# Kernel optimization log

Hardware: AMD Instinct MI355X
Metric: run time of the kernel (lower is better)

## Reference

```python
import jax, jax.numpy as jnp
import numpy as np

N = 50000
E = 400000
IN_DIM = 128
OUT_DIM = 512
NUM_MASK = 15000


def _init_linear(key, din, dout):
    s = 1.0 / np.sqrt(din)
    return jax.random.uniform(key, (din, dout), jnp.float32, -s, s)


def setup_inputs() -> dict:
    key = jax.random.key(0)
    ks = jax.random.split(key, 20)
    attr = jax.random.normal(ks[0], (N, IN_DIM), jnp.float32)
    src = jax.random.randint(ks[1], (E,), 0, N, jnp.int32)
    dst = jax.random.randint(ks[2], (E,), 0, N, jnp.int32)
    mask_nodes = jax.random.randint(ks[3], (NUM_MASK,), 0, N, jnp.int32)
    mask_token = jnp.zeros((1, IN_DIM), jnp.float32)
    dims = [(IN_DIM, OUT_DIM), (OUT_DIM, OUT_DIM), (OUT_DIM, OUT_DIM), (OUT_DIM, IN_DIM)]
    params = {}
    for i, (din, dout) in enumerate(dims, start=1):
        params[f"w_self{i}"] = _init_linear(ks[3 * i + 1], din, dout)
        params[f"w_neigh{i}"] = _init_linear(ks[3 * i + 2], din, dout)
        params[f"b{i}"] = jnp.zeros((dout,), jnp.float32)
    return dict(attr=attr, mask_token=mask_token, src=src, dst=dst, mask_nodes=mask_nodes, **params)


def sage_conv(h, src, dst, w_self, w_neigh, b):
    # mean aggregation over in-neighbors (DGL SAGEConv, aggregator_type='mean')
    msg = h[src]                                              # [E, d]
    agg = jax.ops.segment_sum(msg, dst, num_segments=N)       # [N, d]
    deg = jax.ops.segment_sum(jnp.ones((E,), h.dtype), dst, num_segments=N)
    h_neigh = agg / jnp.maximum(deg, 1.0)[:, None]
    return h @ w_self + h_neigh @ w_neigh + b


def reference(attr, mask_token, src, dst, mask_nodes,
              w_self1, w_neigh1, b1, w_self2, w_neigh2, b2,
              w_self3, w_neigh3, b3, w_self4, w_neigh4, b4):
    # mask node features with the mask token
    h = attr.at[mask_nodes].set(mask_token[0])
    h = jax.nn.relu(sage_conv(h, src, dst, w_self1, w_neigh1, b1))
    h = sage_conv(h, src, dst, w_self2, w_neigh2, b2)          # encoded
    h = jax.nn.relu(sage_conv(h, src, dst, w_self3, w_neigh3, b3))
    decoded = sage_conv(h, src, dst, w_self4, w_neigh4, b4)
    x_orig = attr[mask_nodes]
    x_rec = decoded[mask_nodes]
    return jnp.mean((x_rec - x_orig) ** 2)
```

## Files before the change

### kernel.cpp

```cpp
#include <hip/hip_runtime.h>
#include <cstdint>
#include <cstddef>

#define IN_DIM 128
#define HID    512

typedef unsigned int   uint32;
typedef unsigned short u16;
typedef __attribute__((ext_vector_type(8))) short bf16x8;
typedef __attribute__((ext_vector_type(4))) float f32x4;

static inline int imin_h(int a, int b) { return a < b ? a : b; }

__device__ __forceinline__ float bfu2f(uint32 u) { return __uint_as_float(u << 16); }
__device__ __forceinline__ u16 f2bf(float f) {
  uint32 x = __float_as_uint(f);
  x += 0x7fffu + ((x >> 16) & 1u);
  return (u16)(x >> 16);
}
__device__ __forceinline__ uint32 pack2(float a, float b) {
  return (uint32)f2bf(a) | ((uint32)f2bf(b) << 16);
}

#define GLOBAL_AS(p) ((const __attribute__((address_space(1))) void*)(p))
#define LDS_AS(p)    ((__attribute__((address_space(3))) void*)(p))

__global__ void k_zero2(int* __restrict__ a, int na, int* __restrict__ b, int nb) {
  const int total = na + nb;
  for (int i = blockIdx.x * blockDim.x + threadIdx.x; i < total; i += gridDim.x * blockDim.x) {
    if (i < na) a[i] = 0;
    else        b[i - na] = 0;
  }
}

struct WtJobs {
  const float* W[8];
  u16* Wt[8];
  int K[8];
  int Nn[8];
  int start[9];
};

__global__ __launch_bounds__(256)
void k_prep1(const int* __restrict__ dst, int* __restrict__ deg, int E,
             const float4* __restrict__ attr4, uint2* __restrict__ h0, int n4,
             WtJobs jobs) {
  const int wtot = jobs.start[8];
  const int total = E + n4 + wtot;
  for (int i = blockIdx.x * blockDim.x + threadIdx.x; i < total; i += gridDim.x * blockDim.x) {
    if (i < E) {
      atomicAdd(&deg[dst[i]], 1);
    } else if (i < E + n4) {
      const int t = i - E;
      const float4 v = attr4[t];
      h0[t] = make_uint2(pack2(v.x, v.y), pack2(v.z, v.w));
    } else {
      const int t = i - E - n4;
      int s = 0;
#pragma unroll
      for (int j = 0; j < 7; ++j) s += (t >= jobs.start[j + 1]) ? 1 : 0;
      const int loc = t - jobs.start[s];
      const int K = jobs.K[s], Nn = jobs.Nn[s];
      const int n = loc / K, k = loc - n * K;
      const size_t idx = ((size_t)(n >> 4) * (K >> 5) + (k >> 5)) * 512 +
                         ((k >> 3) & 3) * 128 + ((n & 15) << 3) + (k & 7);
      jobs.Wt[s][idx] = f2bf(jobs.W[s][(size_t)k * Nn + n]);
    }
  }
}

__global__ __launch_bounds__(256)
void k_scan1(const int* __restrict__ deg, int* __restrict__ bsum, int n) {
  __shared__ int sm[256];
  const int base = blockIdx.x * 2048 + threadIdx.x * 8;
  int s = 0;
  if (base + 8 <= n) {
    const uint4 a = *reinterpret_cast<const uint4*>(deg + base);
    const uint4 b = *reinterpret_cast<const uint4*>(deg + base + 4);
    s = (int)(a.x + a.y + a.z + a.w + b.x + b.y + b.z + b.w);
  } else {
    for (int i = 0; i < 8; ++i) if (base + i < n) s += deg[base + i];
  }
  sm[threadIdx.x] = s;
  __syncthreads();
  for (int off = 128; off > 0; off >>= 1) {
    if (threadIdx.x < off) sm[threadIdx.x] += sm[threadIdx.x + off];
    __syncthreads();
  }
  if (threadIdx.x == 0) bsum[blockIdx.x] = sm[0];
}

__global__ __launch_bounds__(256)
void k_scan2(int* __restrict__ bsum, int nb, int* __restrict__ rowptr, int n) {
  __shared__ int sm[256];
  const int v = (threadIdx.x < nb) ? bsum[threadIdx.x] : 0;
  sm[threadIdx.x] = v;
  __syncthreads();
  for (int off = 1; off < 256; off <<= 1) {
    const int t = (threadIdx.x >= off) ? sm[threadIdx.x - off] : 0;
    __syncthreads();
    sm[threadIdx.x] += t;
    __syncthreads();
  }
  if (threadIdx.x < nb) bsum[threadIdx.x] = sm[threadIdx.x] - v;
  if (threadIdx.x == nb - 1) rowptr[n] = sm[threadIdx.x];
}

__global__ __launch_bounds__(256)
void k_scan3(const int* __restrict__ deg, const int* __restrict__ bsum,
             int* __restrict__ rowptr, int* __restrict__ cursor, int n) {
  __shared__ int sm[256];
  const int base = blockIdx.x * 2048 + threadIdx.x * 8;
  int v[8];
  int s = 0;
#pragma unroll
  for (int i = 0; i < 8; ++i) {
    v[i] = (base + i < n) ? deg[base + i] : 0;
    s += v[i];
  }
  sm[threadIdx.x] = s;
  __syncthreads();
  for (int off = 1; off < 256; off <<= 1) {
    const int t = (threadIdx.x >= off) ? sm[threadIdx.x - off] : 0;
    __syncthreads();
    sm[threadIdx.x] += t;
    __syncthreads();
  }
  int run = bsum[blockIdx.x] + sm[threadIdx.x] - s;
#pragma unroll
  for (int i = 0; i < 8; ++i) {
    if (base + i < n) { rowptr[base + i] = run; cursor[base + i] = run; }
    run += v[i];
  }
}

__global__ void k_fillmask(const int* __restrict__ src, const int* __restrict__ dst,
                           int* __restrict__ cursor, int* __restrict__ col, int E,
                           const float4* __restrict__ token, const int* __restrict__ mask,
                           uint2* __restrict__ h0, int NM) {
  const int mtot = NM * (IN_DIM / 4);
  const int total = E + mtot;
  for (int i = blockIdx.x * blockDim.x + threadIdx.x; i < total; i += gridDim.x * blockDim.x) {
    if (i < E) {
      const int p = atomicAdd(&cursor[dst[i]], 1);
      col[p] = src[i];
    } else {
      const int t = i - E;
      const int m = t >> 5;
      const int c = t & 31;
      const float4 tv = token[c];
      h0[(size_t)mask[m] * (IN_DIM / 4) + c] = make_uint2(pack2(tv.x, tv.y), pack2(tv.z, tv.w));
    }
  }
}

template <int D, bool REMAP>
__global__ __launch_bounds__(256)
void k_agg(const u16* __restrict__ h, const int* __restrict__ col,
           const int* __restrict__ rowptr, const int* __restrict__ nodes,
           u16* __restrict__ out, int n) {
  constexpr int V = D / 64;
  const int w = blockIdx.x * (blockDim.x >> 6) + (threadIdx.x >> 6);
  if (w >= n) return;
  const int node = REMAP ? nodes[w] : w;
  const int lane = threadIdx.x & 63;
  const int beg = rowptr[node], end = rowptr[node + 1];
  const size_t loff = (size_t)lane * V;
  float acc[V];
#pragma unroll
  for (int j = 0; j < V; ++j) acc[j] = 0.f;

  if constexpr (V == 8) {
    auto L = [&](int e) {
      return *reinterpret_cast<const uint4*>(h + (size_t)col[e] * D + loff);
    };
    for (int e = beg; e < end; e += 8) {
      uint4 c0{}, c1{}, c2{}, c3{}, c4{}, c5{}, c6{}, c7{};
      c0 = L(e);
      if (e + 1 < end) c1 = L(e + 1);
      if (e + 2 < end) c2 = L(e + 2);
      if (e + 3 < end) c3 = L(e + 3);
      if (e + 4 < end) c4 = L(e + 4);
      if (e + 5 < end) c5 = L(e + 5);
      if (e + 6 < end) c6 = L(e + 6);
      if (e + 7 < end) c7 = L(e + 7);
#define ADD4(cv)                                                      \
      acc[0] += bfu2f(cv.x & 0xffffu); acc[1] += bfu2f(cv.x >> 16);   \
      acc[2] += bfu2f(cv.y & 0xffffu); acc[3] += bfu2f(cv.y >> 16);   \
      acc[4] += bfu2f(cv.z & 0xffffu); acc[5] += bfu2f(cv.z >> 16);   \
      acc[6] += bfu2f(cv.w & 0xffffu); acc[7] += bfu2f(cv.w >> 16);
      ADD4(c0) ADD4(c1) ADD4(c2) ADD4(c3) ADD4(c4) ADD4(c5) ADD4(c6) ADD4(c7)
#undef ADD4
    }
  } else {
    auto L = [&](int e) {
      return *reinterpret_cast<const uint32*>(h + (size_t)col[e] * D + loff);
    };
    for (int e = beg; e < end; e += 8) {
      uint32 c0 = 0, c1 = 0, c2 = 0, c3 = 0, c4 = 0, c5 = 0, c6 = 0, c7 = 0;
      c0 = L(e);
      if (e + 1 < end) c1 = L(e + 1);
      if (e + 2 < end) c2 = L(e + 2);
      if (e + 3 < end) c3 = L(e + 3);
      if (e + 4 < end) c4 = L(e + 4);
      if (e + 5 < end) c5 = L(e + 5);
      if (e + 6 < end) c6 = L(e + 6);
      if (e + 7 < end) c7 = L(e + 7);
#define ADD2(cv) acc[0] += bfu2f(cv & 0xffffu); acc[1] += bfu2f(cv >> 16);
      ADD2(c0) ADD2(c1) ADD2(c2) ADD2(c3) ADD2(c4) ADD2(c5) ADD2(c6) ADD2(c7)
#undef ADD2
    }
  }

  const float inv = 1.0f / fmaxf((float)(end - beg), 1.0f);
  u16* o = out + (size_t)w * D + loff;
  if constexpr (V == 8) {
    uint4 u;
    u.x = pack2(acc[0] * inv, acc[1] * inv);
    u.y = pack2(acc[2] * inv, acc[3] * inv);
    u.z = pack2(acc[4] * inv, acc[5] * inv);
    u.w = pack2(acc[6] * inv, acc[7] * inv);
    *reinterpret_cast<uint4*>(o) = u;
  } else {
    *reinterpret_cast<uint32*>(o) = pack2(acc[0] * inv, acc[1] * inv);
  }
}

template <int DIN, bool RELU>
__global__ __launch_bounds__(512, 4)
void k_gemm_big(const u16* __restrict__ A1, const u16* __restrict__ A2,
                const u16* __restrict__ Wt1, const u16* __restrict__ Wt2,
                const float* __restrict__ bias, u16* __restrict__ out, int M) {
  constexpr int DOUT = HID;
  __shared__ char lds[73728];
  constexpr int KS = DIN / 32;
  constexpr int S  = 2 * KS;
  const int tid = threadIdx.x;
  const int w = tid >> 6, l = tid & 63;
  const int l15 = l & 15, l4 = l >> 4;
  const int wm = w >> 2, wn = w & 3;

  const int nwg  = gridDim.x * gridDim.y;
  const int orig = blockIdx.x + gridDim.x * blockIdx.y;
  const int q = nwg >> 3, r = nwg & 7;
  const int xcd = orig & 7, seq = orig >> 3;
  const int wg = (xcd < r ? xcd * (q + 1) : r * (q + 1) + (xcd - r) * q) + seq;
  const int mt = wg >> 1, nt = wg & 1;
  const int m0 = mt * 128, n0 = nt * 256;

  f32x4 acc[4][4];
#pragma unroll
  for (int i = 0; i < 4; ++i)
#pragma unroll
    for (int j = 0; j < 4; ++j) acc[i][j] = (f32x4){0.f, 0.f, 0.f, 0.f};

  const int arow = min(m0 + w * 16 + l15, M - 1);
  const int kl = l4 * 8;
  const u16* pA1 = A1 + (size_t)arow * DIN + kl;
  const u16* pA2 = A2 + (size_t)arow * DIN + kl;
  const u16* bb1 = Wt1 + ((size_t)(n0 >> 4) + 2 * w) * KS * 512 + (size_t)l * 8;
  const u16* bb2 = Wt2 + ((size_t)(n0 >> 4) + 2 * w) * KS * 512 + (size_t)l * 8;

  auto stage = [&](int s) {
    const int ph = s / KS;
    const int kf = s - ph * KS;
    char* buf = lds + (s % 3) * 24576;
    const u16* a0 = (ph ? pA2 : pA1) + kf * 32;
    const u16* b0 = (ph ? bb2 : bb1) + kf * 512;
    const u16* b1 = b0 + KS * 512;
    __builtin_amdgcn_global_load_lds(GLOBAL_AS(a0), LDS_AS(buf + w * 1024), 16, 0, 0);
    __builtin_amdgcn_global_load_lds(GLOBAL_AS(b0), LDS_AS(buf + 8192 + (2 * w + 0) * 1024), 16, 0, 0);
    __builtin_amdgcn_global_load_lds(GLOBAL_AS(b1), LDS_AS(buf + 8192 + (2 * w + 1) * 1024), 16, 0, 0);
  };

  stage(0);
  stage(1);

#pragma unroll
  for (int s = 0; s < S; ++s) {
    if (s + 1 < S) asm volatile("s_waitcnt vmcnt(3)" ::: "memory");
    else           asm volatile("s_waitcnt vmcnt(0)" ::: "memory");
    __builtin_amdgcn_s_barrier();
    if (s + 2 < S) stage(s + 2);
    char* buf = lds + (s % 3) * 24576;
    bf16x8 af[4], bfr[4];
#pragma unroll
    for (int i = 0; i < 4; ++i)
      af[i] = *reinterpret_cast<const bf16x8*>(buf + (wm * 4 + i) * 1024 + l * 16);
#pragma unroll
    for (int j = 0; j < 4; ++j)
      bfr[j] = *reinterpret_cast<const bf16x8*>(buf + 8192 + (wn * 4 + j) * 1024 + l * 16);
#pragma unroll
    for (int i = 0; i < 4; ++i)
#pragma unroll
      for (int j = 0; j < 4; ++j)
        acc[i][j] = __builtin_amdgcn_mfma_f32_16x16x32_bf16(af[i], bfr[j], acc[i][j], 0, 0, 0);
    asm volatile("s_waitcnt lgkmcnt(0)" ::: "memory");
  }
  __builtin_amdgcn_s_barrier();

  u16* eb = (u16*)(lds + w * 9216);
  float bv[4];
#pragma unroll
  for (int j = 0; j < 4; ++j) bv[j] = bias[n0 + wn * 64 + j * 16 + l15];
#pragma unroll
  for (int i = 0; i < 4; ++i)
#pragma unroll
    for (int j = 0; j < 4; ++j)
#pragma unroll
      for (int r = 0; r < 4; ++r) {
        const int lr = i * 16 + l4 * 4 + r;
        float t = acc[i][j][r] + bv[j];
        if (RELU) t = fmaxf(t, 0.f);
        eb[lr * 72 + j * 16 + l15] = f2bf(t);
      }
  asm volatile("s_waitcnt lgkmcnt(0)" ::: "memory");
#pragma unroll
  for (int p = 0; p < 8; ++p) {
    const int lr = p * 8 + (l >> 3);
    const int row = m0 + wm * 64 + lr;
    if (row < M) {
      const uint4 v = *reinterpret_cast<const uint4*>(eb + lr * 72 + (l & 7) * 8);
      *reinterpret_cast<uint4*>(out + (size_t)row * DOUT + n0 + wn * 64 + (l & 7) * 8) = v;
    }
  }
}

template <int DIN, int DOUT>
__global__ __launch_bounds__(256, 3)
void k_gemm_loss(const u16* __restrict__ A1, const u16* __restrict__ A2,
                 const u16* __restrict__ Wt1, const u16* __restrict__ Wt2,
                 const float* __restrict__ bias, const float* __restrict__ attr,
                 float* __restrict__ partials, int M, const int* __restrict__ remap) {
  __shared__ char lds[49152];
  constexpr int KS = DIN / 32;
  constexpr int S  = 2 * KS;
  const int tid = threadIdx.x;
  const int w = tid >> 6, l = tid & 63;
  const int l15 = l & 15, l4 = l >> 4;
  const int wm = w >> 1, wn = w & 1;

  const int nwg  = gridDim.x * gridDim.y;
  const int orig = blockIdx.x + gridDim.x * blockIdx.y;
  const int q = nwg >> 3, r = nwg & 7;
  const int xcd = orig & 7, seq = orig >> 3;
  const int wg = (xcd < r ? xcd * (q + 1) : r * (q + 1) + (xcd - r) * q) + seq;
  constexpr int NT = DOUT / 128;
  const int mt = wg / NT, nt = wg - mt * NT;
  const int m0 = mt * 128, n0 = nt * 128;

  f32x4 acc[4][4];
#pragma unroll
  for (int i = 0; i < 4; ++i)
#pragma unroll
    for (int j = 0; j < 4; ++j) acc[i][j] = (f32x4){0.f, 0.f, 0.f, 0.f};

  const int am0 = min(m0 + (2 * w) * 16 + l15, M - 1);
  const int am1 = min(m0 + (2 * w + 1) * 16 + l15, M - 1);
  const int ar0 = remap[am0];
  const int ar1 = remap[am1];
  const int kl = l4 * 8;
  const u16* pA1r0 = A1 + (size_t)ar0 * DIN + kl;
  const u16* pA1r1 = A1 + (size_t)ar1 * DIN + kl;
  const u16* pA2r0 = A2 + (size_t)am0 * DIN + kl;
  const u16* pA2r1 = A2 + (size_t)am1 * DIN + kl;
  const u16* bb1 = Wt1 + ((size_t)(n0 >> 4) + 2 * w) * KS * 512 + (size_t)l * 8;
  const u16* bb2 = Wt2 + ((size_t)(n0 >> 4) + 2 * w) * KS * 512 + (size_t)l * 8;

  auto stage = [&](int s) {
    const int ph = s / KS;
    const int kf = s - ph * KS;
    char* buf = lds + (s % 3) * 16384;
    const u16* a0 = (ph ? pA2r0 : pA1r0) + kf * 32;
    const u16* a1 = (ph ? pA2r1 : pA1r1) + kf * 32;
    const u16* b0 = (ph ? bb2 : bb1) + kf * 512;
    const u16* b1 = b0 + KS * 512;
    __builtin_amdgcn_global_load_lds(GLOBAL_AS(a0), LDS_AS(buf + (2 * w + 0) * 1024), 16, 0, 0);
    __builtin_amdgcn_global_load_lds(GLOBAL_AS(a1), LDS_AS(buf + (2 * w + 1) * 1024), 16, 0, 0);
    __builtin_amdgcn_global_load_lds(GLOBAL_AS(b0), LDS_AS(buf + 8192 + (2 * w + 0) * 1024), 16, 0, 0);
    __builtin_amdgcn_global_load_lds(GLOBAL_AS(b1), LDS_AS(buf + 8192 + (2 * w + 1) * 1024), 16, 0, 0);
  };

  stage(0);
  stage(1);

#pragma unroll
  for (int s = 0; s < S; ++s) {
    if (s + 1 < S) asm volatile("s_waitcnt vmcnt(4)" ::: "memory");
    else           asm volatile("s_waitcnt vmcnt(0)" ::: "memory");
    __builtin_amdgcn_s_barrier();
    if (s + 2 < S) stage(s + 2);
    char* buf = lds + (s % 3) * 16384;
    bf16x8 af[4], bfr[4];
#pragma unroll
    for (int i = 0; i < 4; ++i)
      af[i] = *reinterpret_cast<const bf16x8*>(buf + (wm * 4 + i) * 1024 + l * 16);
#pragma unroll
    for (int j = 0; j < 4; ++j)
      bfr[j] = *reinterpret_cast<const bf16x8*>(buf + 8192 + (wn * 4 + j) * 1024 + l * 16);
#pragma unroll
    for (int i = 0; i < 4; ++i)
#pragma unroll
      for (int j = 0; j < 4; ++j)
        acc[i][j] = __builtin_amdgcn_mfma_f32_16x16x32_bf16(af[i], bfr[j], acc[i][j], 0, 0, 0);
    asm volatile("s_waitcnt lgkmcnt(0)" ::: "memory");
  }

  float lsum = 0.f;
#pragma unroll
  for (int j = 0; j < 4; ++j) {
    const int c = n0 + wn * 64 + j * 16 + l15;
    const float bv = bias[c];
#pragma unroll
    for (int i = 0; i < 4; ++i) {
      const int rowb = m0 + wm * 64 + i * 16 + l4 * 4;
#pragma unroll
      for (int r2 = 0; r2 < 4; ++r2) {
        const int row = rowb + r2;
        if (row < M) {
          const float t = bfu2f((uint32)f2bf(acc[i][j][r2] + bv));
          const float d = t - attr[(size_t)remap[row] * IN_DIM + c];
          lsum += d * d;
        }
      }
    }
  }
  __syncthreads();
  float* sm = (float*)lds;
  sm[tid] = lsum;
  __syncthreads();
  for (int off2 = 128; off2 > 0; off2 >>= 1) {
    if (tid < off2) sm[tid] += sm[tid + off2];
    __syncthreads();
  }
  if (tid == 0) atomicAdd(&partials[0], sm[0]);
}

__global__ void k_final(const float* __restrict__ partials, float* __restrict__ out, float inv) {
  out[0] = partials[0] * inv;
}

extern "C" void kernel_launch(void* const* d_in, const int* in_sizes, int n_in,
                              void* d_out, int out_size, void* d_ws, size_t ws_size,
                              hipStream_t stream) {
  const float* attr  = (const float*)d_in[0];
  const float* token = (const float*)d_in[1];
  const int*   src   = (const int*)d_in[2];
  const int*   dst   = (const int*)d_in[3];
  const int*   mask  = (const int*)d_in[4];
  const float* Wself[4]  = {(const float*)d_in[5], (const float*)d_in[8],
                            (const float*)d_in[11], (const float*)d_in[14]};
  const float* Wneigh[4] = {(const float*)d_in[6], (const float*)d_in[9],
                            (const float*)d_in[12], (const float*)d_in[15]};
  const float* Bias[4]   = {(const float*)d_in[7], (const float*)d_in[10],
                            (const float*)d_in[13], (const float*)d_in[16]};
  const int N  = in_sizes[0] / IN_DIM;
  const int E  = in_sizes[2];
  const int NM = in_sizes[4];

  size_t off = 0;
  auto take = [&](size_t bytes) -> void* {
    void* p = (char*)d_ws + off;
    off += (bytes + 255) & ~(size_t)255;
    return p;
  };
  u16* HA = (u16*)take((size_t)N * HID * sizeof(u16));
  u16* HB = (u16*)take((size_t)N * HID * sizeof(u16));
  const int dims_in[4]  = {IN_DIM, HID, HID, HID};
  const int dims_out[4] = {HID, HID, HID, IN_DIM};
  u16* WtS[4]; u16* WtN[4];
  for (int i = 0; i < 4; ++i) {
    WtS[i] = (u16*)take((size_t)dims_in[i] * dims_out[i] * sizeof(u16));
    WtN[i] = (u16*)take((size_t)dims_in[i] * dims_out[i] * sizeof(u16));
  }
  int* deg    = (int*)take((size_t)N * sizeof(int));
  int* rowptr = (int*)take((size_t)(N + 1) * sizeof(int));
  int* cursor = (int*)take((size_t)N * sizeof(int));
  int* col    = (int*)take((size_t)E * sizeof(int));
  int* bsum   = (int*)take(256 * sizeof(int));
  float* partials = (float*)take(512 * sizeof(float));

  size_t rem = (ws_size > off + 4096) ? (ws_size - off - 4096) : 0;
  const int cap = (int)(rem / ((size_t)HID * sizeof(u16)));
  const int want = (N + 255) & ~255;
  int chunk = (cap >= want) ? want : (cap & ~255);
  if (chunk < 2048) chunk = 2048;
  u16* CH = (u16*)take((size_t)chunk * HID * sizeof(u16));

  k_zero2<<<imin_h((N + 512 + 255) / 256, 1024), 256, 0, stream>>>(deg, N, (int*)partials, 512);

  WtJobs jobs;
  int acc0 = 0;
  for (int i = 0; i < 4; ++i) {
    jobs.W[2 * i] = Wself[i];  jobs.Wt[2 * i] = WtS[i];
    jobs.K[2 * i] = dims_in[i]; jobs.Nn[2 * i] = dims_out[i];
    jobs.start[2 * i] = acc0;   acc0 += dims_in[i] * dims_out[i];
    jobs.W[2 * i + 1] = Wneigh[i]; jobs.Wt[2 * i + 1] = WtN[i];
    jobs.K[2 * i + 1] = dims_in[i]; jobs.Nn[2 * i + 1] = dims_out[i];
    jobs.start[2 * i + 1] = acc0;  acc0 += dims_in[i] * dims_out[i];
  }
  jobs.start[8] = acc0;
  const int n4 = N * (IN_DIM / 4);
  const int p1 = E + n4 + acc0;
  k_prep1<<<imin_h((p1 + 255) / 256, 4096), 256, 0, stream>>>(
      dst, deg, E, (const float4*)attr, (uint2*)HA, n4, jobs);

  const int nb = (N + 2047) / 2048;
  k_scan1<<<nb, 256, 0, stream>>>(deg, bsum, N);
  k_scan2<<<1, 256, 0, stream>>>(bsum, nb, rowptr, N);
  k_scan3<<<nb, 256, 0, stream>>>(deg, bsum, rowptr, cursor, N);

  const int p2 = E + NM * (IN_DIM / 4);
  k_fillmask<<<imin_h((p2 + 255) / 256, 4096), 256, 0, stream>>>(
      src, dst, cursor, col, E, (const float4*)token, mask, (uint2*)HA, NM);

  auto run_layer = [&](const u16* hin, u16* hout, int din, int layer, bool relu) {
    for (int c0 = 0; c0 < N; c0 += chunk) {
      const int mc = imin_h(chunk, N - c0);
      const int ab = (mc + 3) / 4;
      if (din == IN_DIM)
        k_agg<IN_DIM, false><<<ab, 256, 0, stream>>>(hin, col, rowptr + c0, nullptr, CH, mc);
      else
        k_agg<HID, false><<<ab, 256, 0, stream>>>(hin, col, rowptr + c0, nullptr, CH, mc);
      const u16* a1 = hin + (size_t)c0 * din;
      u16* o = hout + (size_t)c0 * HID;
      const int mb = (mc + 127) / 128;
      if (din == IN_DIM && relu)
        k_gemm_big<IN_DIM, true><<<dim3(2, mb), 512, 0, stream>>>(
            a1, CH, WtS[layer], WtN[layer], Bias[layer], o, mc);
      else if (relu)
        k_gemm_big<HID, true><<<dim3(2, mb), 512, 0, stream>>>(
            a1, CH, WtS[layer], WtN[layer], Bias[layer], o, mc);
      else
        k_gemm_big<HID, false><<<dim3(2, mb), 512, 0, stream>>>(
            a1, CH, WtS[layer], WtN[layer], Bias[layer], o, mc);
    }
  };

  run_layer(HA, HB, IN_DIM, 0, true);
  run_layer(HB, HA, HID,    1, false);
  run_layer(HA, HB, HID,    2, true);

  k_agg<HID, true><<<(NM + 3) / 4, 256, 0, stream>>>(HB, col, rowptr, mask, CH, NM);
  k_gemm_loss<HID, IN_DIM><<<dim3(1, (NM + 127) / 128), 256, 0, stream>>>(
      HB, CH, WtS[3], WtN[3], Bias[3], attr, partials, NM, mask);

  k_final<<<1, 1, 0, stream>>>(partials, (float*)d_out, 1.0f / ((float)NM * IN_DIM));
}
```

Measured before the change: 431.4 us.

## Switch big GEMM to 32x32x16 MFMA with matching weight layout

Rewrites the main layer GEMM to use 32x32x16 bf16 MFMA tiles instead of 16x16x32. Each wave now holds a 2x2 grid of 32x32 accumulators, and the A and B LDS fragment layouts change to match. Weights are pre-transposed into a new 32-column blocked layout. Separate copies in the old 16-row layout are added for the loss GEMM, which still uses the smaller instruction. The aim is fewer MFMA issues and LDS reads per FLOP, at the cost of extra weight-preparation work and a more complex epilogue index mapping.

```diff
diff --git a/kernel.cpp b/kernel.cpp
--- a/kernel.cpp
+++ b/kernel.cpp
@@ -7,8 +7,9 @@
 
 typedef unsigned int   uint32;
 typedef unsigned short u16;
-typedef __attribute__((ext_vector_type(8))) short bf16x8;
-typedef __attribute__((ext_vector_type(4))) float f32x4;
+typedef __attribute__((ext_vector_type(8)))  short bf16x8;
+typedef __attribute__((ext_vector_type(4)))  float f32x4;
+typedef __attribute__((ext_vector_type(16))) float f32x16;
 
 static inline int imin_h(int a, int b) { return a < b ? a : b; }
 
@@ -34,18 +35,19 @@
 }
 
 struct WtJobs {
-  const float* W[8];
-  u16* Wt[8];
-  int K[8];
-  int Nn[8];
-  int start[9];
+  const float* W[10];
+  u16* Wt[10];
+  int K[10];
+  int Nn[10];
+  int mode[10];
+  int start[11];
 };
 
 __global__ __launch_bounds__(256)
 void k_prep1(const int* __restrict__ dst, int* __restrict__ deg, int E,
              const float4* __restrict__ attr4, uint2* __restrict__ h0, int n4,
              WtJobs jobs) {
-  const int wtot = jobs.start[8];
+  const int wtot = jobs.start[10];
   const int total = E + n4 + wtot;
   for (int i = blockIdx.x * blockDim.x + threadIdx.x; i < total; i += gridDim.x * blockDim.x) {
     if (i < E) {
@@ -58,12 +60,17 @@
       const int t = i - E - n4;
       int s = 0;
 #pragma unroll
-      for (int j = 0; j < 7; ++j) s += (t >= jobs.start[j + 1]) ? 1 : 0;
+      for (int j = 0; j < 9; ++j) s += (t >= jobs.start[j + 1]) ? 1 : 0;
       const int loc = t - jobs.start[s];
       const int K = jobs.K[s], Nn = jobs.Nn[s];
       const int n = loc / K, k = loc - n * K;
-      const size_t idx = ((size_t)(n >> 4) * (K >> 5) + (k >> 5)) * 512 +
-                         ((k >> 3) & 3) * 128 + ((n & 15) << 3) + (k & 7);
+      size_t idx;
+      if (jobs.mode[s] == 0)
+        idx = ((size_t)(n >> 5) * (K >> 4) + (k >> 4)) * 512 +
+              ((k >> 3) & 1) * 256 + ((n & 31) << 3) + (k & 7);
+      else
+        idx = ((size_t)(n >> 4) * (K >> 5) + (k >> 5)) * 512 +
+              ((k >> 3) & 3) * 128 + ((n & 15) << 3) + (k & 7);
       jobs.Wt[s][idx] = f2bf(jobs.W[s][(size_t)k * Nn + n]);
     }
   }
@@ -233,11 +240,12 @@
                 const float* __restrict__ bias, u16* __restrict__ out, int M) {
   constexpr int DOUT = HID;
   __shared__ char lds[73728];
-  constexpr int KS = DIN / 32;
-  constexpr int S  = 2 * KS;
+  constexpr int KS   = DIN / 32;
+  constexpr int S    = 2 * KS;
+  constexpr int KS16 = DIN / 16;
   const int tid = threadIdx.x;
   const int w = tid >> 6, l = tid & 63;
-  const int l15 = l & 15, l4 = l >> 4;
+  const int l31 = l & 31, l5 = l >> 5;
   const int wm = w >> 2, wn = w & 3;
 
   const int nwg  = gridDim.x * gridDim.y;
@@ -248,29 +256,30 @@
   const int mt = wg >> 1, nt = wg & 1;
   const int m0 = mt * 128, n0 = nt * 256;
 
-  f32x4 acc[4][4];
-#pragma unroll
-  for (int i = 0; i < 4; ++i)
-#pragma unroll
-    for (int j = 0; j < 4; ++j) acc[i][j] = (f32x4){0.f, 0.f, 0.f, 0.f};
-
-  const int arow = min(m0 + w * 16 + l15, M - 1);
-  const int kl = l4 * 8;
-  const u16* pA1 = A1 + (size_t)arow * DIN + kl;
-  const u16* pA2 = A2 + (size_t)arow * DIN + kl;
-  const u16* bb1 = Wt1 + ((size_t)(n0 >> 4) + 2 * w) * KS * 512 + (size_t)l * 8;
-  const u16* bb2 = Wt2 + ((size_t)(n0 >> 4) + 2 * w) * KS * 512 + (size_t)l * 8;
+  f32x16 acc[2][2];
+#pragma unroll
+  for (int i = 0; i < 2; ++i)
+#pragma unroll
+    for (int j = 0; j < 2; ++j)
+#pragma unroll
+      for (int r2 = 0; r2 < 16; ++r2) acc[i][j][r2] = 0.f;
+
+  const int arow = min(m0 + (w >> 1) * 32 + l31, M - 1);
+  const int kA = (w & 1) * 16 + l5 * 8;
+  const u16* pA1 = A1 + (size_t)arow * DIN + kA;
+  const u16* pA2 = A2 + (size_t)arow * DIN + kA;
+  const u16* bb1 = Wt1 + ((size_t)(n0 >> 5) + w) * KS16 * 512 + (size_t)l * 8;
+  const u16* bb2 = Wt2 + ((size_t)(n0 >> 5) + w) * KS16 * 512 + (size_t)l * 8;
 
   auto stage = [&](int s) {
     const int ph = s / KS;
     const int kf = s - ph * KS;
     char* buf = lds + (s % 3) * 24576;
-    const u16* a0 = (ph ? pA2 : pA1) + kf * 32;
-    const u16* b0 = (ph ? bb2 : bb1) + kf * 512;
-    const u16* b1 = b0 + KS * 512;
-    __builtin_amdgcn_global_load_lds(GLOBAL_AS(a0), LDS_AS(buf + w * 1024), 16, 0, 0);
-    __builtin_amdgcn_global_load_lds(GLOBAL_AS(b0), LDS_AS(buf + 8192 + (2 * w + 0) * 1024), 16, 0, 0);
-    __builtin_amdgcn_global_load_lds(GLOBAL_AS(b1), LDS_AS(buf + 8192 + (2 * w + 1) * 1024), 16, 0, 0);
+    const u16* a = (ph ? pA2 : pA1) + kf * 32;
+    const u16* b = (ph ? bb2 : bb1) + (size_t)(kf * 2) * 512;
+    __builtin_amdgcn_global_load_lds(GLOBAL_AS(a),       LDS_AS(buf + w * 1024), 16, 0, 0);
+    __builtin_amdgcn_global_load_lds(GLOBAL_AS(b),       LDS_AS(buf + 8192 + (2 * w + 0) * 1024), 16, 0, 0);
+    __builtin_amdgcn_global_load_lds(GLOBAL_AS(b + 512), LDS_AS(buf + 8192 + (2 * w + 1) * 1024), 16, 0, 0);
   };
 
   stage(0);
@@ -283,36 +292,42 @@
     __builtin_amdgcn_s_barrier();
     if (s + 2 < S) stage(s + 2);
     char* buf = lds + (s % 3) * 24576;
-    bf16x8 af[4], bfr[4];
-#pragma unroll
-    for (int i = 0; i < 4; ++i)
-      af[i] = *reinterpret_cast<const bf16x8*>(buf + (wm * 4 + i) * 1024 + l * 16);
-#pragma unroll
-    for (int j = 0; j < 4; ++j)
-      bfr[j] = *reinterpret_cast<const bf16x8*>(buf + 8192 + (wn * 4 + j) * 1024 + l * 16);
-#pragma unroll
-    for (int i = 0; i < 4; ++i)
-#pragma unroll
-      for (int j = 0; j < 4; ++j)
-        acc[i][j] = __builtin_amdgcn_mfma_f32_16x16x32_bf16(af[i], bfr[j], acc[i][j], 0, 0, 0);
+    bf16x8 af[2][2], bfr[2][2];
+#pragma unroll
+    for (int i = 0; i < 2; ++i)
+#pragma unroll
+      for (int kk = 0; kk < 2; ++kk)
+        af[i][kk] = *reinterpret_cast<const bf16x8*>(buf + ((wm * 2 + i) * 2 + kk) * 1024 + l * 16);
+#pragma unroll
+    for (int j = 0; j < 2; ++j)
+#pragma unroll
+      for (int kk = 0; kk < 2; ++kk)
+        bfr[j][kk] = *reinterpret_cast<const bf16x8*>(buf + 8192 + ((wn * 2 + j) * 2 + kk) * 1024 + l * 16);
+#pragma unroll
+    for (int kk = 0; kk < 2; ++kk)
+#pragma unroll
+      for (int i = 0; i < 2; ++i)
+#pragma unroll
+        for (int j = 0; j < 2; ++j)
+          acc[i][j] = __builtin_amdgcn_mfma_f32_32x32x16_bf16(af[i][kk], bfr[j][kk], acc[i][j], 0, 0, 0);
     asm volatile("s_waitcnt lgkmcnt(0)" ::: "memory");
   }
   __builtin_amdgcn_s_barrier();
 
   u16* eb = (u16*)(lds + w * 9216);
-  float bv[4];
-#pragma unroll
-  for (int j = 0; j < 4; ++j) bv[j] = bias[n0 + wn * 64 + j * 16 + l15];
-#pragma unroll
-  for (int i = 0; i < 4; ++i)
-#pragma unroll
-    for (int j = 0; j < 4; ++j)
-#pragma unroll
-      for (int r = 0; r < 4; ++r) {
-        const int lr = i * 16 + l4 * 4 + r;
-        float t = acc[i][j][r] + bv[j];
+  float bv[2];
+#pragma unroll
+  for (int j = 0; j < 2; ++j) bv[j] = bias[n0 + wn * 64 + j * 32 + l31];
+#pragma unroll
+  for (int i = 0; i < 2; ++i)
+#pragma unroll
+    for (int j = 0; j < 2; ++j)
+#pragma unroll
+      for (int r2 = 0; r2 < 16; ++r2) {
+        const int lr = i * 32 + (r2 & 3) + 8 * (r2 >> 2) + 4 * l5;
+        float t = acc[i][j][r2] + bv[j];
         if (RELU) t = fmaxf(t, 0.f);
-        eb[lr * 72 + j * 16 + l15] = f2bf(t);
+        eb[lr * 72 + j * 32 + l31] = f2bf(t);
       }
   asm volatile("s_waitcnt lgkmcnt(0)" ::: "memory");
 #pragma unroll
@@ -473,6 +488,8 @@
     WtS[i] = (u16*)take((size_t)dims_in[i] * dims_out[i] * sizeof(u16));
     WtN[i] = (u16*)take((size_t)dims_in[i] * dims_out[i] * sizeof(u16));
   }
+  u16* WtS16_3 = (u16*)take((size_t)HID * IN_DIM * sizeof(u16));
+  u16* WtN16_3 = (u16*)take((size_t)HID * IN_DIM * sizeof(u16));
   int* deg    = (int*)take((size_t)N * sizeof(int));
   int* rowptr = (int*)take((size_t)(N + 1) * sizeof(int));
   int* cursor = (int*)take((size_t)N * sizeof(int));
@@ -493,13 +510,17 @@
   int acc0 = 0;
   for (int i = 0; i < 4; ++i) {
     jobs.W[2 * i] = Wself[i];  jobs.Wt[2 * i] = WtS[i];
-    jobs.K[2 * i] = dims_in[i]; jobs.Nn[2 * i] = dims_out[i];
+    jobs.K[2 * i] = dims_in[i]; jobs.Nn[2 * i] = dims_out[i]; jobs.mode[2 * i] = 0;
     jobs.start[2 * i] = acc0;   acc0 += dims_in[i] * dims_out[i];
     jobs.W[2 * i + 1] = Wneigh[i]; jobs.Wt[2 * i + 1] = WtN[i];
-    jobs.K[2 * i + 1] = dims_in[i]; jobs.Nn[2 * i + 1] = dims_out[i];
+    jobs.K[2 * i + 1] = dims_in[i]; jobs.Nn[2 * i + 1] = dims_out[i]; jobs.mode[2 * i + 1] = 0;
     jobs.start[2 * i + 1] = acc0;  acc0 += dims_in[i] * dims_out[i];
   }
-  jobs.start[8] = acc0;
+  jobs.W[8] = Wself[3];  jobs.Wt[8] = WtS16_3; jobs.K[8] = HID; jobs.Nn[8] = IN_DIM;
+  jobs.mode[8] = 1; jobs.start[8] = acc0; acc0 += HID * IN_DIM;
+  jobs.W[9] = Wneigh[3]; jobs.Wt[9] = WtN16_3; jobs.K[9] = HID; jobs.Nn[9] = IN_DIM;
+  jobs.mode[9] = 1; jobs.start[9] = acc0; acc0 += HID * IN_DIM;
+  jobs.start[10] = acc0;
   const int n4 = N * (IN_DIM / 4);
   const int p1 = E + n4 + acc0;
   k_prep1<<<imin_h((p1 + 255) / 256, 4096), 256, 0, stream>>>(
@@ -543,7 +564,7 @@
 
   k_agg<HID, true><<<(NM + 3) / 4, 256, 0, stream>>>(HB, col, rowptr, mask, CH, NM);
   k_gemm_loss<HID, IN_DIM><<<dim3(1, (NM + 127) / 128), 256, 0, stream>>>(
-      HB, CH, WtS[3], WtN[3], Bias[3], attr, partials, NM, mask);
+      HB, CH, WtS16_3, WtN16_3, Bias[3], attr, partials, NM, mask);
 
   k_final<<<1, 1, 0, stream>>>(partials, (float*)d_out, 1.0f / ((float)NM * IN_DIM));
 }
```

New measurement: 442.1 us (median of 3 runs). 1.02x slower.
